# Kernel optimization log

Hardware: AMD Instinct MI355X
Metric: run time of the kernel (lower is better)

The kernel has to match this reference:

```python
import jax, jax.numpy as jnp
import numpy as np

N = 8192
D_IN = 128
D_OUT = 64
NEG_SLOPE = 0.2
MASK_VAL = -9e15


def setup_inputs() -> dict:
    key = jax.random.key(0)
    k_in, k_adj, k_w, k_a = jax.random.split(key, 4)
    inp = jax.random.normal(k_in, (1, N, D_IN), dtype=jnp.float32)
    adj = jax.random.uniform(k_adj, (N, N), dtype=jnp.float32)
    # xavier_uniform with gain=1.414
    gain = 1.414
    bw = gain * np.sqrt(6.0 / (D_IN + D_OUT))
    w = jax.random.uniform(k_w, (D_IN, D_OUT), dtype=jnp.float32, minval=-bw, maxval=bw)
    ba = gain * np.sqrt(6.0 / (2 * D_OUT + 1))
    a = jax.random.uniform(k_a, (2 * D_OUT, 1), dtype=jnp.float32, minval=-ba, maxval=ba)
    a_coeff = jnp.ones((1,), dtype=jnp.float32)
    b_coeff = jnp.ones((1,), dtype=jnp.float32)
    return {"input": inp, "adj": adj, "w": w, "a": a, "a_coeff": a_coeff, "b_coeff": b_coeff}


def reference(input, adj, w, a, a_coeff, b_coeff):
    h = input[0] @ w                      # [N, D_OUT]
    # e[i,j] = [h_i, h_j] . a  ==  (h @ a1)_i + (h @ a2)_j  (fused, no N^2*2D concat)
    a1 = a[:D_OUT, 0]
    a2 = a[D_OUT:, 0]
    e = (h @ a1)[:, None] + (h @ a2)[None, :]             # [N, N]
    adj_t = a_coeff[0] * adj + b_coeff[0]
    lrelu = jnp.where(adj_t >= 0, adj_t, NEG_SLOPE * adj_t)
    e_t = lrelu * e
    attn = jnp.where(adj > 0, e_t, jnp.float32(MASK_VAL))
    attn = jax.nn.softmax(attn, axis=1)                    # masked row softmax
    h_prime = attn @ h                                     # [N, D_OUT]
    return jax.nn.elu(h_prime)                             # concat=True -> elu
```

## Files before the change

### kernel.cpp

```cpp
#include <hip/hip_runtime.h>

#define NN 8192
#define DIN 128
#define DOUT 64

typedef __attribute__((ext_vector_type(8))) short short8;
typedef __attribute__((ext_vector_type(4))) float f32x4;

static __device__ __forceinline__ unsigned short f2bf(float x) {
  unsigned u = __builtin_bit_cast(unsigned, x);
  u = (u + 0x7FFFu + ((u >> 16) & 1u)) >> 16;
  return (unsigned short)u;
}

__global__ __launch_bounds__(256) void k_h(
    const float* __restrict__ x, const float* __restrict__ wmat,
    const float* __restrict__ avec, float* __restrict__ f,
    float* __restrict__ g, unsigned short* __restrict__ hbf) {
  const int t = threadIdx.x;
  const int lane = t & 63;
  const int row = blockIdx.x * 4 + (t >> 6);
  const float* xr = x + (size_t)row * DIN;
  float acc = 0.f;
#pragma unroll 8
  for (int k = 0; k < DIN; ++k) acc = fmaf(xr[k], wmat[k * DOUT + lane], acc);

  float fa = acc * avec[lane];
  float ga = acc * avec[DOUT + lane];
#pragma unroll
  for (int off = 32; off; off >>= 1) {
    fa += __shfl_xor(fa, off);
    ga += __shfl_xor(ga, off);
  }
  if (lane == 0) { f[row] = fa; g[row] = ga; }

  const int jt  = row >> 5;
  const int grp = (row >> 3) & 3;
  const int e   = row & 7;
  const int ns  = lane >> 4;
  const int l15 = lane & 15;
  hbf[((size_t)(jt * 4 + ns) * 64 + grp * 16 + l15) * 8 + e] = f2bf(acc);
}

__global__ __launch_bounds__(256) void k_main(
    const float* __restrict__ adj, const float* __restrict__ f,
    const float* __restrict__ g, const unsigned short* __restrict__ hbf,
    const float* __restrict__ acp, const float* __restrict__ bcp,
    float* __restrict__ out) {
  const int t = threadIdx.x;
  const int wv = t >> 6, lane = t & 63;
  const int r = lane & 15, grp = lane >> 4;
  const int i0 = blockIdx.x * 16;
  const float ac = acp[0], bc = bcp[0];
  const float fr = f[i0 + r];
  const float L2E = 1.4426950408889634f;
  const float MASKV = -9.0e15f;

  float m = MASKV, s = 0.f;
  f32x4 acc0 = {0.f, 0.f, 0.f, 0.f};
  f32x4 acc1 = acc0, acc2 = acc0, acc3 = acc0;

  const float* arow = adj + (size_t)(i0 + r) * NN;

  for (int jt = wv; jt < NN / 32; jt += 4) {
    const int jb = jt * 32 + grp * 8;
    const float4 A0 = *reinterpret_cast<const float4*>(arow + jb);
    const float4 A1 = *reinterpret_cast<const float4*>(arow + jb + 4);
    const float4 G0 = *reinterpret_cast<const float4*>(g + jb);
    const float4 G1 = *reinterpret_cast<const float4*>(g + jb + 4);
    const short8* bp = reinterpret_cast<const short8*>(hbf) + (size_t)jt * 256 + lane;
    const short8 B0 = bp[0], B1 = bp[64], B2 = bp[128], B3 = bp[192];

    const float av[8] = {A0.x, A0.y, A0.z, A0.w, A1.x, A1.y, A1.z, A1.w};
    const float gv[8] = {G0.x, G0.y, G0.z, G0.w, G1.x, G1.y, G1.z, G1.w};
    float sc[8];
    float tmax = MASKV;
#pragma unroll
    for (int e = 0; e < 8; ++e) {
      const float adjv = av[e];
      const float tl = fmaf(ac, adjv, bc);
      const float lr = fmaxf(tl, 0.2f * tl);
      float sv = lr * (fr + gv[e]);
      sv = adjv > 0.f ? sv : MASKV;
      sc[e] = sv;
      tmax = fmaxf(tmax, sv);
    }
    tmax = fmaxf(tmax, __shfl_xor(tmax, 16));
    tmax = fmaxf(tmax, __shfl_xor(tmax, 32));

    if (__any(tmax > m + 8.f)) {
      const float mn = fmaxf(m, tmax);
      const float scale = exp2f((m - mn) * L2E);
      s *= scale;
      const float s0 = __shfl(scale, grp * 4 + 0);
      const float s1 = __shfl(scale, grp * 4 + 1);
      const float s2 = __shfl(scale, grp * 4 + 2);
      const float s3 = __shfl(scale, grp * 4 + 3);
      const f32x4 sv4 = {s0, s1, s2, s3};
      acc0 *= sv4; acc1 *= sv4; acc2 *= sv4; acc3 *= sv4;
      m = mn;
    }

    const float mL = m * L2E;
    short8 afrag;
    float ps = 0.f;
#pragma unroll
    for (int e = 0; e < 8; ++e) {
      const float p = exp2f(fmaf(sc[e], L2E, -mL));
      ps += p;
      afrag[e] = (short)f2bf(p);
    }
    s += ps;

    acc0 = __builtin_amdgcn_mfma_f32_16x16x32_bf16(afrag, B0, acc0, 0, 0, 0);
    acc1 = __builtin_amdgcn_mfma_f32_16x16x32_bf16(afrag, B1, acc1, 0, 0, 0);
    acc2 = __builtin_amdgcn_mfma_f32_16x16x32_bf16(afrag, B2, acc2, 0, 0, 0);
    acc3 = __builtin_amdgcn_mfma_f32_16x16x32_bf16(afrag, B3, acc3, 0, 0, 0);
  }

  s += __shfl_xor(s, 16);
  s += __shfl_xor(s, 32);

  __shared__ float sm[4][16];
  __shared__ float ssum[4][16];
  __shared__ float sacc[4][16][65];
  if (grp == 0) { sm[wv][r] = m; ssum[wv][r] = s; }
#pragma unroll
  for (int reg = 0; reg < 4; ++reg) {
    sacc[wv][grp * 4 + reg][ 0 + r] = acc0[reg];
    sacc[wv][grp * 4 + reg][16 + r] = acc1[reg];
    sacc[wv][grp * 4 + reg][32 + r] = acc2[reg];
    sacc[wv][grp * 4 + reg][48 + r] = acc3[reg];
  }
  __syncthreads();

  const int c = t & 63;
#pragma unroll
  for (int rr = 0; rr < 4; ++rr) {
    const int row = (t >> 6) * 4 + rr;
    const float M = fmaxf(fmaxf(sm[0][row], sm[1][row]),
                          fmaxf(sm[2][row], sm[3][row]));
    float S = 0.f, A = 0.f;
#pragma unroll
    for (int k = 0; k < 4; ++k) {
      const float e = exp2f((sm[k][row] - M) * L2E);
      S += ssum[k][row] * e;
      A += sacc[k][row][c] * e;
    }
    const float v = A / S;
    out[(size_t)(i0 + row) * DOUT + c] = v > 0.f ? v : expm1f(v);
  }
}

extern "C" void kernel_launch(void* const* d_in, const int* in_sizes, int n_in,
                              void* d_out, int out_size, void* d_ws, size_t ws_size,
                              hipStream_t stream) {
  const float* x    = (const float*)d_in[0];
  const float* adj  = (const float*)d_in[1];
  const float* wmat = (const float*)d_in[2];
  const float* avec = (const float*)d_in[3];
  const float* acp  = (const float*)d_in[4];
  const float* bcp  = (const float*)d_in[5];
  float* out = (float*)d_out;

  float* f = (float*)d_ws;
  float* g = f + NN;
  unsigned short* hbf = (unsigned short*)(g + NN);

  k_h<<<NN / 4, 256, 0, stream>>>(x, wmat, avec, f, g, hbf);
  k_main<<<NN / 16, 256, 0, stream>>>(adj, f, g, hbf, acp, bcp, out);
}
```

Measured before the change: 99.09 us.

## Split attention columns across two blocks per row stripe and prefetch adj

Each 16-row stripe is now handled by two blocks, each covering half of the column tiles. The grid doubles from 512 to 1024 blocks, which gives more parallelism over the 8192x8192 adj stream on the MI355X's CUs. Each block writes partial (max, sum, accumulator) values to workspace, and a new combine kernel merges the two halves and applies the normalisation and ELU. The adj loads are also software-prefetched one iteration ahead, with a launch_bounds occupancy hint added. The cost is an extra kernel launch, an extra round trip of partial results through global memory, and higher register pressure from the prefetch.

```diff
diff --git a/kernel.cpp b/kernel.cpp
--- a/kernel.cpp
+++ b/kernel.cpp
@@ -42,15 +42,17 @@
   hbf[((size_t)(jt * 4 + ns) * 64 + grp * 16 + l15) * 8 + e] = f2bf(acc);
 }
 
-__global__ __launch_bounds__(256) void k_main(
+__global__ __launch_bounds__(256, 4) void k_main(
     const float* __restrict__ adj, const float* __restrict__ f,
     const float* __restrict__ g, const unsigned short* __restrict__ hbf,
     const float* __restrict__ acp, const float* __restrict__ bcp,
-    float* __restrict__ out) {
+    float* __restrict__ pacc, float* __restrict__ pms) {
   const int t = threadIdx.x;
   const int wv = t >> 6, lane = t & 63;
   const int r = lane & 15, grp = lane >> 4;
-  const int i0 = blockIdx.x * 16;
+  const int stripe = blockIdx.x >> 1;
+  const int half = blockIdx.x & 1;
+  const int i0 = stripe * 16;
   const float ac = acp[0], bc = bcp[0];
   const float fr = f[i0 + r];
   const float L2E = 1.4426950408889634f;
@@ -61,11 +63,18 @@
   f32x4 acc1 = acc0, acc2 = acc0, acc3 = acc0;
 
   const float* arow = adj + (size_t)(i0 + r) * NN;
-
-  for (int jt = wv; jt < NN / 32; jt += 4) {
+  const int jtEnd = half * 128 + 128;
+
+  int jt0 = half * 128 + wv;
+  float4 A0 = *reinterpret_cast<const float4*>(arow + jt0 * 32 + grp * 8);
+  float4 A1 = *reinterpret_cast<const float4*>(arow + jt0 * 32 + grp * 8 + 4);
+
+  for (int jt = jt0; jt < jtEnd; jt += 4) {
+    const int jn = (jt + 4 < jtEnd) ? jt + 4 : jt;
+    const float4 nA0 = *reinterpret_cast<const float4*>(arow + jn * 32 + grp * 8);
+    const float4 nA1 = *reinterpret_cast<const float4*>(arow + jn * 32 + grp * 8 + 4);
+
     const int jb = jt * 32 + grp * 8;
-    const float4 A0 = *reinterpret_cast<const float4*>(arow + jb);
-    const float4 A1 = *reinterpret_cast<const float4*>(arow + jb + 4);
     const float4 G0 = *reinterpret_cast<const float4*>(g + jb);
     const float4 G1 = *reinterpret_cast<const float4*>(g + jb + 4);
     const short8* bp = reinterpret_cast<const short8*>(hbf) + (size_t)jt * 256 + lane;
@@ -116,6 +125,8 @@
     acc1 = __builtin_amdgcn_mfma_f32_16x16x32_bf16(afrag, B1, acc1, 0, 0, 0);
     acc2 = __builtin_amdgcn_mfma_f32_16x16x32_bf16(afrag, B2, acc2, 0, 0, 0);
     acc3 = __builtin_amdgcn_mfma_f32_16x16x32_bf16(afrag, B3, acc3, 0, 0, 0);
+
+    A0 = nA0; A1 = nA1;
   }
 
   s += __shfl_xor(s, 16);
@@ -135,6 +146,8 @@
   __syncthreads();
 
   const int c = t & 63;
+  float* paccB = pacc + (size_t)blockIdx.x * 16 * 64;
+  float* pmsB  = pms  + (size_t)blockIdx.x * 32;
 #pragma unroll
   for (int rr = 0; rr < 4; ++rr) {
     const int row = (t >> 6) * 4 + rr;
@@ -147,9 +160,29 @@
       S += ssum[k][row] * e;
       A += sacc[k][row][c] * e;
     }
-    const float v = A / S;
-    out[(size_t)(i0 + row) * DOUT + c] = v > 0.f ? v : expm1f(v);
-  }
+    paccB[row * 64 + c] = A;
+    if (c == 0) { pmsB[row * 2] = M; pmsB[row * 2 + 1] = S; }
+  }
+}
+
+__global__ __launch_bounds__(256) void k_comb(
+    const float* __restrict__ pacc, const float* __restrict__ pms,
+    float* __restrict__ out) {
+  const int idx = blockIdx.x * 256 + threadIdx.x;
+  const int row = idx >> 6, c = idx & 63;
+  const int stripe = row >> 4, rin = row & 15;
+  const float L2E = 1.4426950408889634f;
+  const size_t b0 = (size_t)stripe * 2, b1 = b0 + 1;
+  const float m0 = pms[b0 * 32 + rin * 2], s0 = pms[b0 * 32 + rin * 2 + 1];
+  const float m1 = pms[b1 * 32 + rin * 2], s1 = pms[b1 * 32 + rin * 2 + 1];
+  const float M = fmaxf(m0, m1);
+  const float e0 = exp2f((m0 - M) * L2E);
+  const float e1 = exp2f((m1 - M) * L2E);
+  const float A = pacc[b0 * 1024 + rin * 64 + c] * e0 +
+                  pacc[b1 * 1024 + rin * 64 + c] * e1;
+  const float S = s0 * e0 + s1 * e1;
+  const float v = A / S;
+  out[idx] = v > 0.f ? v : expm1f(v);
 }
 
 extern "C" void kernel_launch(void* const* d_in, const int* in_sizes, int n_in,
@@ -166,7 +199,10 @@
   float* f = (float*)d_ws;
   float* g = f + NN;
   unsigned short* hbf = (unsigned short*)(g + NN);
+  float* pacc = (float*)(hbf + (size_t)NN * DOUT);
+  float* pms  = pacc + (size_t)1024 * 16 * 64;
 
   k_h<<<NN / 4, 256, 0, stream>>>(x, wmat, avec, f, g, hbf);
-  k_main<<<NN / 16, 256, 0, stream>>>(adj, f, g, hbf, acp, bcp, out);
-}
+  k_main<<<NN / 8, 256, 0, stream>>>(adj, f, g, hbf, acp, bcp, pacc, pms);
+  k_comb<<<NN * DOUT / 256, 256, 0, stream>>>(pacc, pms, out);
+}
```

Result: no change. 97.28 us (-1.8%).
